# Optimization experiments

Measured on AMD Instinct MI355X. Metric: run time of the kernel, lower is better.

Reference implementation:

```python
import jax, jax.numpy as jnp
import numpy as np

# Module config (matches init_kwargs shape_data=[8,32,32], pow=1, spde_type='adv_diff')
N_T, N_Y, N_X = 8, 32, 32
N = N_Y * N_X            # nb_nodes
DX = DY = DT = 1.0


def build_A(kappa, m1, m2, h11, h12, h22):
    """Dense [N,N] advection-diffusion operator A = kappa^2 I + m.grad - div(H grad),
    central differences on the n_y x n_x grid, zero-Dirichlet boundary (9-pt stencil).
    All coefficient inputs are [N] vectors (node-wise)."""
    ii, jj = jnp.divmod(jnp.arange(N), N_X)   # ii: y index, jj: x index
    rows = jnp.arange(N)
    A = jnp.zeros((N, N), dtype=kappa.dtype)
    # center
    A = A.at[rows, rows].add(kappa ** 2 + 2.0 * h11 / DX**2 + 2.0 * h22 / DY**2)

    def add(A, di, dj, coef):
        vi, vj = ii + di, jj + dj
        valid = (vi >= 0) & (vi < N_Y) & (vj >= 0) & (vj < N_X)
        cols = jnp.clip(vi, 0, N_Y - 1) * N_X + jnp.clip(vj, 0, N_X - 1)
        return A.at[rows, cols].add(jnp.where(valid, coef, 0.0))

    A = add(A, 0, +1, -h11 / DX**2 + m1 / (2.0 * DX))
    A = add(A, 0, -1, -h11 / DX**2 - m1 / (2.0 * DX))
    A = add(A, +1, 0, -h22 / DY**2 + m2 / (2.0 * DY))
    A = add(A, -1, 0, -h22 / DY**2 - m2 / (2.0 * DY))
    cxy = h12 / (2.0 * DX * DY)    # cross term -2*H12*u_xy with /(4 dx dy) stencil
    A = add(A, +1, +1, -cxy)
    A = add(A, -1, -1, -cxy)
    A = add(A, +1, -1, +cxy)
    A = add(A, -1, +1, +cxy)
    return A


def _forward(kappa, m, H, tau):
    n_b = kappa.shape[0]
    # reorder field params to [n_b, n_t, N]
    kap = jnp.moveaxis(kappa[:, 0], -1, 1)
    m1 = jnp.moveaxis(m[:, 0], -1, 1)
    m2 = jnp.moveaxis(m[:, 1], -1, 1)
    h11 = jnp.moveaxis(H[:, 0, 0], -1, 1)
    h12 = jnp.moveaxis(H[:, 0, 1], -1, 1)
    h22 = jnp.moveaxis(H[:, 1, 1], -1, 1)
    tau_ = jnp.moveaxis(tau[:, 0], -1, 1)

    flat = lambda a: a.reshape(n_b * N_T, N)
    A = jax.vmap(build_A)(flat(kap), flat(m1), flat(m2), flat(h11), flat(h12), flat(h22))
    A = A.reshape(n_b, N_T, N, N)                 # B = A since pow == 1

    eye = jnp.eye(N, dtype=A.dtype)
    M = eye + DT * A                               # inv_M_k = I + dt*B_k, [n_b,n_t,N,N]
    w = DT / (tau_ ** 2)                           # Qs_tilde_k = diag(dt / tau_k^2)

    WM = w[..., :, None] * M                       # diag(w_k) @ M_k
    P = jnp.einsum('btij,btik->btjk', M, WM)       # M_k^T diag(w_k) M_k

    # diagonal blocks: D_k = P_k + diag(w_{k+1}) for k < n_t-1; D_{n_t-1} = P_{n_t-1}
    w_next = jnp.concatenate([w[:, 1:], jnp.zeros_like(w[:, :1])], axis=1)
    D = P + w_next[..., :, None] * eye

    # sub-diagonal block (k, k-1) = -M_k^T diag(w_k), k = 1..n_t-1 (0-block padded at front)
    zblk = jnp.zeros((n_b, 1, N, N), dtype=A.dtype)
    lower = jnp.concatenate([zblk, -jnp.swapaxes(WM[:, 1:], -1, -2)], axis=1)
    # super-diagonal block (k, k+1) = -diag(w_{k+1}) M_{k+1}, k = 0..n_t-2 (0-block at end)
    upper = jnp.concatenate([-WM[:, 1:], zblk], axis=1)

    # block-tridiagonal precision Q, packed as [n_b, 3(diag,lower,upper), n_t, N, N]
    return jnp.stack([D, lower, upper], axis=1)


def setup_inputs() -> dict:
    key = jax.random.key(0)
    ks = jax.random.split(key, 4)
    n_b = 2
    kappa = 0.1 + 0.9 * jax.random.uniform(ks[0], (n_b, 1, N, N_T), dtype=jnp.float32)
    m = 0.2 * jax.random.normal(ks[1], (n_b, 2, N, N_T), dtype=jnp.float32)
    H = jax.random.uniform(ks[2], (n_b, 2, 2, N, N_T), dtype=jnp.float32)
    H = H.at[:, 0, 1].multiply(0.2)
    H = H.at[:, 1, 0].set(H[:, 0, 1])              # symmetric diffusion tensor
    tau = 0.5 + jax.random.uniform(ks[3], (n_b, 1, N, N_T), dtype=jnp.float32)
    return {"kappa": kappa, "m": m, "H": H, "tau": tau}


def reference(kappa, m, H, tau):
    return _forward(kappa, m, H, tau)
```

## Files before the change

### kernel.cpp

```cpp
#include <hip/hip_runtime.h>

#define NT 8
#define NY 32
#define NX 32
#define NN 1024

__device__ __forceinline__ void node_coefs(const float* __restrict__ kap,
                                           const float* __restrict__ m,
                                           const float* __restrict__ H,
                                           const float* __restrict__ tau,
                                           int b, int node, int tc,
                                           int iy, int ix,
                                           float* c , float& w) {
    const int base = node * NT + tc;
    const float kp  = kap[(b * NN) * NT + base];
    const float m1  = m[((b * 2 + 0) * NN) * NT + base];
    const float m2  = m[((b * 2 + 1) * NN) * NT + base];
    const float h11 = H[((b * 4 + 0) * NN) * NT + base];
    const float h12 = H[((b * 4 + 1) * NN) * NT + base];
    const float h22 = H[((b * 4 + 3) * NN) * NT + base];
    const float tv  = tau[(b * NN) * NT + base];
    w = 1.0f / (tv * tv);

    const float cxy = 0.5f * h12;
    const bool ym = iy > 0, yp = iy < NY - 1;
    const bool xm = ix > 0, xp = ix < NX - 1;

    c[4] = 1.0f + kp * kp + 2.0f * h11 + 2.0f * h22;
    c[0] = (ym && xm) ? -cxy               : 0.0f;
    c[1] =  ym        ? (-h22 - 0.5f * m2) : 0.0f;
    c[2] = (ym && xp) ?  cxy               : 0.0f;
    c[3] =  xm        ? (-h11 - 0.5f * m1) : 0.0f;
    c[5] =  xp        ? (-h11 + 0.5f * m1) : 0.0f;
    c[6] = (yp && xm) ?  cxy               : 0.0f;
    c[7] =  yp        ? (-h22 + 0.5f * m2) : 0.0f;
    c[8] = (yp && xp) ? -cxy               : 0.0f;
}

__global__ __launch_bounds__(1024) void precompute_kernel(
        const float* __restrict__ kap, const float* __restrict__ m,
        const float* __restrict__ H, const float* __restrict__ tau,
        float* __restrict__ U, float* __restrict__ D0) {
    __shared__ float sc[NN][9];
    __shared__ float sw[NN];

    const int bt = blockIdx.x;
    const int b = bt >> 3, t = bt & 7;
    const int j = threadIdx.x;
    const int jy = j >> 5, jx = j & 31;

    float c[9], w;
    node_coefs(kap, m, H, tau, b, j, t, jy, jx, c, w);

    {
        float* up = U + ((size_t)bt * NN + j) * 9;
        #pragma unroll
        for (int q = 0; q < 9; ++q) up[q] = -w * c[q];
    }
    #pragma unroll
    for (int q = 0; q < 9; ++q) sc[j][q] = c[q];
    sw[j] = w;
    __syncthreads();

    float wnext = 0.0f;
    if (t < NT - 1) {
        const float tv = tau[((size_t)b * NN + j) * NT + (t + 1)];
        wnext = 1.0f / (tv * tv);
    }

    float* dp = D0 + ((size_t)bt * NN + j) * 25;
    #pragma unroll
    for (int dy = -2; dy <= 2; ++dy) {
        #pragma unroll
        for (int dx = -2; dx <= 2; ++dx) {
            float acc = 0.0f;
            #pragma unroll
            for (int d = 0; d < 9; ++d) {
                const int ey = d / 3 - 1, ex = d % 3 - 1;
                const int r2y = dy - ey, r2x = dx - ex;
                if (r2y < -1 || r2y > 1 || r2x < -1 || r2x > 1) continue;
                const int iy = jy + ey, ix = jx + ex;
                if (iy < 0 || iy >= NY || ix < 0 || ix >= NX) continue;
                const int jn = iy * NX + ix;
                acc += sw[jn] * sc[jn][8 - d] * sc[jn][(r2y + 1) * 3 + (r2x + 1)];
            }
            if (dy == 0 && dx == 0) acc += wnext;
            dp[(dy + 2) * 5 + (dx + 2)] = acc;
        }
    }
}

__global__ __launch_bounds__(256) void writer_kernel(
        const float* __restrict__ U, const float* __restrict__ D0,
        float* __restrict__ out) {
    const unsigned gid = blockIdx.x * 256u + threadIdx.x;
    const unsigned row = gid >> 8;
    const unsigned q   = gid & 255u;

    const int j   = row & (NN - 1);
    const int t   = (row >> 10) & 7;
    const int bb  = row >> 13;
    const int blk = bb % 3;
    const int b   = bb / 3;
    const int jy = j >> 5, jx = j & 31;
    const int cy = q >> 3;
    const int cx0 = (q & 7) * 4;

    float4 v = make_float4(0.f, 0.f, 0.f, 0.f);
    float* vp = &v.x;
    const int ddy = cy - jy;

    if (blk == 0) {
        if (ddy >= -2 && ddy <= 2) {
            const float* base = D0 + ((size_t)(b * NT + t) * NN + j) * 25
                                   + (ddy + 2) * 5;
            #pragma unroll
            for (int qq = 0; qq < 4; ++qq) {
                const int ddx = cx0 + qq - jx;
                if (ddx >= -2 && ddx <= 2) vp[qq] = base[ddx + 2];
            }
        }
    } else if (blk == 1) {
        if (t > 0 && ddy >= -1 && ddy <= 1) {
            #pragma unroll
            for (int qq = 0; qq < 4; ++qq) {
                const int ddx = cx0 + qq - jx;
                if (ddx >= -1 && ddx <= 1) {
                    const int k = (cy * NX) + (cx0 + qq);
                    const int off = (ddy + 1) * 3 + (ddx + 1);
                    vp[qq] = U[((size_t)(b * NT + t) * NN + k) * 9 + (8 - off)];
                }
            }
        }
    } else {
        if (t < NT - 1 && ddy >= -1 && ddy <= 1) {
            const float* up = U + ((size_t)(b * NT + t + 1) * NN + j) * 9
                                + (ddy + 1) * 3;
            #pragma unroll
            for (int qq = 0; qq < 4; ++qq) {
                const int ddx = cx0 + qq - jx;
                if (ddx >= -1 && ddx <= 1) vp[qq] = up[ddx + 1];
            }
        }
    }

    float4* op = (float4*)out;
    op[gid] = v;
}

extern "C" void kernel_launch(void* const* d_in, const int* in_sizes, int n_in,
                              void* d_out, int out_size, void* d_ws, size_t ws_size,
                              hipStream_t stream) {
    const float* kap = (const float*)d_in[0];
    const float* m   = (const float*)d_in[1];
    const float* H   = (const float*)d_in[2];
    const float* tau = (const float*)d_in[3];
    float* out = (float*)d_out;

    const int n_b = in_sizes[0] / (NN * NT);

    float* U  = (float*)d_ws;
    float* D0 = U + (size_t)n_b * NT * NN * 9;

    precompute_kernel<<<n_b * NT, 1024, 0, stream>>>(kap, m, H, tau, U, D0);

    const unsigned total_quads = (unsigned)n_b * 3u * NT * NN * (NN / 4);
    writer_kernel<<<total_quads / 256u, 256, 0, stream>>>(U, D0, out);
}
```

Baseline: 212.3 us.

## Restructure precompute without shared memory and make writer grid-stride with nontemporal stores

```diff
diff --git a/kernel.cpp b/kernel.cpp
--- a/kernel.cpp
+++ b/kernel.cpp
@@ -4,6 +4,8 @@
 #define NY 32
 #define NX 32
 #define NN 1024
+
+typedef float v4f __attribute__((ext_vector_type(4)));
 
 __device__ __forceinline__ void node_coefs(const float* __restrict__ kap,
                                            const float* __restrict__ m,
@@ -37,115 +39,138 @@
     c[8] = (yp && xp) ? -cxy               : 0.0f;
 }
 
-__global__ __launch_bounds__(1024) void precompute_kernel(
+__global__ __launch_bounds__(256) void precompute_kernel(
         const float* __restrict__ kap, const float* __restrict__ m,
         const float* __restrict__ H, const float* __restrict__ tau,
         float* __restrict__ U, float* __restrict__ D0) {
-    __shared__ float sc[NN][9];
-    __shared__ float sw[NN];
-
-    const int bt = blockIdx.x;
+    const int gtid = blockIdx.x * 256 + threadIdx.x;
+    const int j  = gtid & (NN - 1);
+    const int bt = gtid >> 10;
     const int b = bt >> 3, t = bt & 7;
-    const int j = threadIdx.x;
     const int jy = j >> 5, jx = j & 31;
 
-    float c[9], w;
-    node_coefs(kap, m, H, tau, b, j, t, jy, jx, c, w);
+    float acc[25];
+    #pragma unroll
+    for (int q = 0; q < 25; ++q) acc[q] = 0.0f;
 
-    {
-        float* up = U + ((size_t)bt * NN + j) * 9;
-        #pragma unroll
-        for (int q = 0; q < 9; ++q) up[q] = -w * c[q];
+    #pragma unroll
+    for (int d = 0; d < 9; ++d) {
+        const int ey = d / 3 - 1, ex = d % 3 - 1;
+        const int iy = jy + ey, ix = jx + ex;
+        if (iy >= 0 && iy < NY && ix >= 0 && ix < NX) {
+            float c[9], w;
+            node_coefs(kap, m, H, tau, b, iy * NX + ix, t, iy, ix, c, w);
+            const float wmj = w * c[8 - d];
+            #pragma unroll
+            for (int r2 = 0; r2 < 9; ++r2) {
+                const int ry = r2 / 3 - 1, rx = r2 % 3 - 1;
+                acc[(ey + ry + 2) * 5 + (ex + rx + 2)] += wmj * c[r2];
+            }
+            if (d == 4) {
+                float* up = U + ((size_t)bt * NN + j) * 9;
+                #pragma unroll
+                for (int q = 0; q < 9; ++q) up[q] = -w * c[q];
+            }
+        }
     }
-    #pragma unroll
-    for (int q = 0; q < 9; ++q) sc[j][q] = c[q];
-    sw[j] = w;
-    __syncthreads();
-
-    float wnext = 0.0f;
     if (t < NT - 1) {
         const float tv = tau[((size_t)b * NN + j) * NT + (t + 1)];
-        wnext = 1.0f / (tv * tv);
+        acc[12] += 1.0f / (tv * tv);
     }
-
     float* dp = D0 + ((size_t)bt * NN + j) * 25;
     #pragma unroll
-    for (int dy = -2; dy <= 2; ++dy) {
-        #pragma unroll
-        for (int dx = -2; dx <= 2; ++dx) {
-            float acc = 0.0f;
-            #pragma unroll
-            for (int d = 0; d < 9; ++d) {
-                const int ey = d / 3 - 1, ex = d % 3 - 1;
-                const int r2y = dy - ey, r2x = dx - ex;
-                if (r2y < -1 || r2y > 1 || r2x < -1 || r2x > 1) continue;
-                const int iy = jy + ey, ix = jx + ex;
-                if (iy < 0 || iy >= NY || ix < 0 || ix >= NX) continue;
-                const int jn = iy * NX + ix;
-                acc += sw[jn] * sc[jn][8 - d] * sc[jn][(r2y + 1) * 3 + (r2x + 1)];
-            }
-            if (dy == 0 && dx == 0) acc += wnext;
-            dp[(dy + 2) * 5 + (dx + 2)] = acc;
-        }
-    }
+    for (int q = 0; q < 25; ++q) dp[q] = acc[q];
 }
 
 __global__ __launch_bounds__(256) void writer_kernel(
         const float* __restrict__ U, const float* __restrict__ D0,
-        float* __restrict__ out) {
-    const unsigned gid = blockIdx.x * 256u + threadIdx.x;
-    const unsigned row = gid >> 8;
-    const unsigned q   = gid & 255u;
+        float* __restrict__ out, int ngroups) {
+    const int tid = threadIdx.x;
+    const int cy  = tid >> 3;
+    const int cx0 = (tid & 7) * 4;
+    const v4f z = {0.f, 0.f, 0.f, 0.f};
 
-    const int j   = row & (NN - 1);
-    const int t   = (row >> 10) & 7;
-    const int bb  = row >> 13;
-    const int blk = bb % 3;
-    const int b   = bb / 3;
-    const int jy = j >> 5, jx = j & 31;
-    const int cy = q >> 3;
-    const int cx0 = (q & 7) * 4;
+    for (int g = blockIdx.x; g < ngroups; g += gridDim.x) {
+        const int row0 = g << 2;
+        const int j0  = row0 & (NN - 1);
+        const int t   = (row0 >> 10) & 7;
+        const int bb  = row0 >> 13;
+        const int blk = bb % 3;
+        const int b   = bb / 3;
+        const int jy = j0 >> 5, jx0 = j0 & 31;
+        v4f* op = (v4f*)out + ((size_t)row0 << 8) + tid;
 
-    float4 v = make_float4(0.f, 0.f, 0.f, 0.f);
-    float* vp = &v.x;
-    const int ddy = cy - jy;
+        if ((blk == 1 && t == 0) || (blk == 2 && t == NT - 1)) {
+            __builtin_nontemporal_store(z, op);
+            __builtin_nontemporal_store(z, op + 256);
+            __builtin_nontemporal_store(z, op + 512);
+            __builtin_nontemporal_store(z, op + 768);
+            continue;
+        }
 
-    if (blk == 0) {
-        if (ddy >= -2 && ddy <= 2) {
-            const float* base = D0 + ((size_t)(b * NT + t) * NN + j) * 25
-                                   + (ddy + 2) * 5;
-            #pragma unroll
-            for (int qq = 0; qq < 4; ++qq) {
-                const int ddx = cx0 + qq - jx;
-                if (ddx >= -2 && ddx <= 2) vp[qq] = base[ddx + 2];
+        const int ddy = cy - jy;
+        float v[16];
+        #pragma unroll
+        for (int q = 0; q < 16; ++q) v[q] = 0.0f;
+
+        if (blk == 0) {
+            if (ddy >= -2 && ddy <= 2) {
+                const float* dbase = D0 + ((size_t)(b * NT + t) * NN + j0) * 25
+                                        + (ddy + 2) * 5 + 2;
+                #pragma unroll
+                for (int r = 0; r < 4; ++r) {
+                    const int jx = jx0 + r;
+                    #pragma unroll
+                    for (int qq = 0; qq < 4; ++qq) {
+                        const int ddx = cx0 + qq - jx;
+                        if (ddx >= -2 && ddx <= 2) v[r * 4 + qq] = dbase[r * 25 + ddx];
+                    }
+                }
             }
-        }
-    } else if (blk == 1) {
-        if (t > 0 && ddy >= -1 && ddy <= 1) {
-            #pragma unroll
-            for (int qq = 0; qq < 4; ++qq) {
-                const int ddx = cx0 + qq - jx;
-                if (ddx >= -1 && ddx <= 1) {
-                    const int k = (cy * NX) + (cx0 + qq);
-                    const int off = (ddy + 1) * 3 + (ddx + 1);
-                    vp[qq] = U[((size_t)(b * NT + t) * NN + k) * 9 + (8 - off)];
+        } else if (blk == 1) {
+            if (ddy >= -1 && ddy <= 1) {
+                const float* ub = U + (size_t)(b * NT + t) * NN * 9;
+                #pragma unroll
+                for (int r = 0; r < 4; ++r) {
+                    const int jx = jx0 + r;
+                    #pragma unroll
+                    for (int qq = 0; qq < 4; ++qq) {
+                        const int ddx = cx0 + qq - jx;
+                        if (ddx >= -1 && ddx <= 1) {
+                            const int k = cy * NX + cx0 + qq;
+                            const int off = (ddy + 1) * 3 + (ddx + 1);
+                            v[r * 4 + qq] = ub[(size_t)k * 9 + (8 - off)];
+                        }
+                    }
+                }
+            }
+        } else {
+            if (ddy >= -1 && ddy <= 1) {
+                const float* ub = U + ((size_t)(b * NT + t + 1) * NN + j0) * 9
+                                    + (ddy + 1) * 3 + 1;
+                #pragma unroll
+                for (int r = 0; r < 4; ++r) {
+                    const int jx = jx0 + r;
+                    #pragma unroll
+                    for (int qq = 0; qq < 4; ++qq) {
+                        const int ddx = cx0 + qq - jx;
+                        if (ddx >= -1 && ddx <= 1) v[r * 4 + qq] = ub[r * 9 + ddx];
+                    }
                 }
             }
         }
-    } else {
-        if (t < NT - 1 && ddy >= -1 && ddy <= 1) {
-            const float* up = U + ((size_t)(b * NT + t + 1) * NN + j) * 9
-                                + (ddy + 1) * 3;
-            #pragma unroll
-            for (int qq = 0; qq < 4; ++qq) {
-                const int ddx = cx0 + qq - jx;
-                if (ddx >= -1 && ddx <= 1) vp[qq] = up[ddx + 1];
-            }
+
+        {
+            v4f a = {v[0], v[1], v[2], v[3]};
+            v4f bq = {v[4], v[5], v[6], v[7]};
+            v4f cq = {v[8], v[9], v[10], v[11]};
+            v4f dq = {v[12], v[13], v[14], v[15]};
+            __builtin_nontemporal_store(a,  op);
+            __builtin_nontemporal_store(bq, op + 256);
+            __builtin_nontemporal_store(cq, op + 512);
+            __builtin_nontemporal_store(dq, op + 768);
         }
     }
-
-    float4* op = (float4*)out;
-    op[gid] = v;
 }
 
 extern "C" void kernel_launch(void* const* d_in, const int* in_sizes, int n_in,
@@ -162,8 +187,9 @@
     float* U  = (float*)d_ws;
     float* D0 = U + (size_t)n_b * NT * NN * 9;
 
-    precompute_kernel<<<n_b * NT, 1024, 0, stream>>>(kap, m, H, tau, U, D0);
+    precompute_kernel<<<n_b * NT * NN / 256, 256, 0, stream>>>(kap, m, H, tau, U, D0);
 
-    const unsigned total_quads = (unsigned)n_b * 3u * NT * NN * (NN / 4);
-    writer_kernel<<<total_quads / 256u, 256, 0, stream>>>(U, D0, out);
+    const int ngroups = n_b * 3 * NT * NN / 4;
+    const int grid = ngroups < 4096 ? ngroups : 4096;
+    writer_kernel<<<grid, 256, 0, stream>>>(U, D0, out, ngroups);
 }
```

New measurement: 217.7 us. 1.03x slower.
